# Kernel tuning notes

Measured on AMD Instinct MI355X. Metric: run time of the kernel, lower is better.

The kernel has to match this reference:

```python
import math
import jax, jax.numpy as jnp
import numpy as np

DIM = 768
TARGET_DIM = 1024  # next power of two >= DIM


def _hadamard_matrix(n: int) -> np.ndarray:
    # Sylvester construction, normalized by 1/sqrt(n)
    H = np.array([[1.0]], dtype=np.float32)
    while H.shape[0] < n:
        H = np.block([[H, H], [H, -H]])
    return H / math.sqrt(n)


_H = jnp.asarray(_hadamard_matrix(TARGET_DIM))  # [1024, 1024]


def setup_inputs() -> dict:
    key = jax.random.key(0)
    x = jax.random.normal(key, (16, 768, 56, 56), dtype=jnp.float32)
    return {"x": x}


def reference(x):
    B, C, Hs, Ws = x.shape  # C == DIM
    # [B, C, H, W] -> [B, H, W, C] -> [B*H*W, C]
    xr = jnp.transpose(x, (0, 2, 3, 1)).reshape(-1, DIM)
    # pad channel dim up to TARGET_DIM
    xp = jnp.pad(xr, ((0, 0), (0, TARGET_DIM - DIM)))
    y = xp @ _H.astype(x.dtype)           # [B*H*W, 1024]
    y = y[:, :DIM]                        # slice back to dim
    y = y.reshape(B, Hs, Ws, C)
    return jnp.transpose(y, (0, 3, 1, 2))  # [B, C, H, W]
```

## Files before the change

kernel.cpp:

```cpp
#include <hip/hip_runtime.h>


#define NSPAT 3136
#define TS    32
#define STQ   33
#define STI   529

static __device__ __forceinline__ float2 f2add(float2 a, float2 b) {
    return make_float2(a.x + b.x, a.y + b.y);
}
static __device__ __forceinline__ float2 f2sub(float2 a, float2 b) {
    return make_float2(a.x - b.x, a.y - b.y);
}

#define FWHT_STAGE(arr, D)                                   \
    _Pragma("unroll")                                        \
    for (int _b = 0; _b < 32; _b += 2 * (D)) {               \
        _Pragma("unroll")                                    \
        for (int _k = 0; _k < (D); ++_k) {                   \
            float2 _t = arr[_b + _k];                        \
            arr[_b + _k]       = f2add(_t, arr[_b + _k + (D)]); \
            arr[_b + _k + (D)] = f2sub(_t, arr[_b + _k + (D)]); \
        }                                                    \
    }

#define FWHT32(arr)       \
    FWHT_STAGE(arr, 16)   \
    FWHT_STAGE(arr, 8)    \
    FWHT_STAGE(arr, 4)    \
    FWHT_STAGE(arr, 2)    \
    FWHT_STAGE(arr, 1)

__global__ __launch_bounds__(256, 2)
void hadamard_c768_kernel(const float* __restrict__ x, float* __restrict__ y) {
    __shared__ float lds[24 * STI];

    const int t   = threadIdx.x;
    const int s2  = t & 15;
    const int g   = t >> 4;
    const int bid = blockIdx.x;
    const int b   = bid / (NSPAT / TS);
    const int s0  = (bid % (NSPAT / TS)) * TS;

    const int base = b * 768 * NSPAT + s0 + 2 * s2;
    const float* xb = x + base;
    float*       yb = y + base;

    float2 a0[32], a1[32];
    #pragma unroll
    for (int j = 0; j < 32; ++j)
        a0[j] = *(const float2*)(xb + (32 * g + j) * NSPAT);
    FWHT32(a0)

    const bool twoRows = (g < 8);
    if (twoRows) {
        #pragma unroll
        for (int j = 0; j < 32; ++j)
            a1[j] = *(const float2*)(xb + (32 * (g + 16) + j) * NSPAT);
        FWHT32(a1)
    }

    #pragma unroll
    for (int round = 0; round < 2; ++round) {
        const int qbase = 16 * round;

        {
            float* p = lds + g * STI + 2 * s2;
            #pragma unroll
            for (int qq = 0; qq < 16; ++qq) {
                p[qq * STQ]     = a0[qbase + qq].x;
                p[qq * STQ + 1] = a0[qbase + qq].y;
            }
            if (twoRows) {
                float* p1 = lds + (g + 16) * STI + 2 * s2;
                #pragma unroll
                for (int qq = 0; qq < 16; ++qq) {
                    p1[qq * STQ]     = a1[qbase + qq].x;
                    p1[qq * STQ + 1] = a1[qbase + qq].y;
                }
            }
        }
        __syncthreads();

        {
            float2 w[32];
            const float* p = lds + g * STQ + 2 * s2;
            #pragma unroll
            for (int i = 0; i < 24; ++i)
                w[i] = make_float2(p[i * STI], p[i * STI + 1]);

            #pragma unroll
            for (int i = 0; i < 8; ++i) {
                float2 tt = w[i];
                w[i]      = f2add(tt, w[i + 16]);
                w[i + 16] = f2sub(tt, w[i + 16]);
            }
            #pragma unroll
            for (int i = 8; i < 16; ++i)
                w[i + 16] = w[i];

            FWHT_STAGE(w, 8)
            FWHT_STAGE(w, 4)
            FWHT_STAGE(w, 2)
            FWHT_STAGE(w, 1)

            const int q = qbase + g;
            #pragma unroll
            for (int pp = 0; pp < 24; ++pp) {
                float2 v = w[pp];
                v.x *= 0.03125f;
                v.y *= 0.03125f;
                *(float2*)(yb + (32 * pp + q) * NSPAT) = v;
            }
        }
        if (round == 0)
            __syncthreads();
    }
}

extern "C" void kernel_launch(void* const* d_in, const int* in_sizes, int n_in,
                              void* d_out, int out_size, void* d_ws, size_t ws_size,
                              hipStream_t stream) {
    const float* x = (const float*)d_in[0];
    float*       y = (float*)d_out;
    const int nblocks = 16 * (NSPAT / TS);
    hadamard_c768_kernel<<<dim3(nblocks), dim3(256), 0, stream>>>(x, y);
}
```

Measured before the change: 272.6 us.

## Use 512 threads per block with one row group each and nontemporal scalar stores

Blocks grow from 256 to 512 threads. Each of 24 active 16-lane groups loads and transforms one 32-channel row group, which removes the uneven two-row-group work of the old layout. The second stage now uses scalar floats: each thread handles one spatial column for one q, and the output goes through nontemporal stores. This raises occupancy and balances work, at the cost of a quarter of the threads sitting idle in the first phase and narrower scalar stores in place of float2 stores.

```diff
diff --git a/kernel.cpp b/kernel.cpp
--- a/kernel.cpp
+++ b/kernel.cpp
@@ -13,7 +13,7 @@
     return make_float2(a.x - b.x, a.y - b.y);
 }
 
-#define FWHT_STAGE(arr, D)                                   \
+#define FWHT_STAGE2(arr, D)                                  \
     _Pragma("unroll")                                        \
     for (int _b = 0; _b < 32; _b += 2 * (D)) {               \
         _Pragma("unroll")                                    \
@@ -24,96 +24,92 @@
         }                                                    \
     }
 
-#define FWHT32(arr)       \
-    FWHT_STAGE(arr, 16)   \
-    FWHT_STAGE(arr, 8)    \
-    FWHT_STAGE(arr, 4)    \
-    FWHT_STAGE(arr, 2)    \
-    FWHT_STAGE(arr, 1)
+#define FWHT32_2(arr)      \
+    FWHT_STAGE2(arr, 16)   \
+    FWHT_STAGE2(arr, 8)    \
+    FWHT_STAGE2(arr, 4)    \
+    FWHT_STAGE2(arr, 2)    \
+    FWHT_STAGE2(arr, 1)
 
-__global__ __launch_bounds__(256, 2)
+#define FWHT_STAGE1(arr, D)                                  \
+    _Pragma("unroll")                                        \
+    for (int _b = 0; _b < 32; _b += 2 * (D)) {               \
+        _Pragma("unroll")                                    \
+        for (int _k = 0; _k < (D); ++_k) {                   \
+            float _t = arr[_b + _k];                         \
+            arr[_b + _k]       = _t + arr[_b + _k + (D)];    \
+            arr[_b + _k + (D)] = _t - arr[_b + _k + (D)];    \
+        }                                                    \
+    }
+
+__global__ __launch_bounds__(512, 5)
 void hadamard_c768_kernel(const float* __restrict__ x, float* __restrict__ y) {
     __shared__ float lds[24 * STI];
 
     const int t   = threadIdx.x;
-    const int s2  = t & 15;
-    const int g   = t >> 4;
     const int bid = blockIdx.x;
     const int b   = bid / (NSPAT / TS);
     const int s0  = (bid % (NSPAT / TS)) * TS;
+    const int base = b * 768 * NSPAT + s0;
 
-    const int base = b * 768 * NSPAT + s0 + 2 * s2;
-    const float* xb = x + base;
-    float*       yb = y + base;
+    const int g  = t >> 4;
+    const int ln = t & 15;
 
-    float2 a0[32], a1[32];
-    #pragma unroll
-    for (int j = 0; j < 32; ++j)
-        a0[j] = *(const float2*)(xb + (32 * g + j) * NSPAT);
-    FWHT32(a0)
-
-    const bool twoRows = (g < 8);
-    if (twoRows) {
+    float2 a[32];
+    const bool active = (g < 24);
+    if (active) {
+        const float* xb = x + base + 2 * ln;
         #pragma unroll
         for (int j = 0; j < 32; ++j)
-            a1[j] = *(const float2*)(xb + (32 * (g + 16) + j) * NSPAT);
-        FWHT32(a1)
+            a[j] = *(const float2*)(xb + (32 * g + j) * NSPAT);
+        FWHT32_2(a)
     }
 
+    const int q16 = t >> 5;
+    const int s   = t & 31;
+
     #pragma unroll
-    for (int round = 0; round < 2; ++round) {
-        const int qbase = 16 * round;
-
-        {
-            float* p = lds + g * STI + 2 * s2;
+    for (int r = 0; r < 2; ++r) {
+        if (active) {
+            float* p = lds + g * STI + 2 * ln;
             #pragma unroll
             for (int qq = 0; qq < 16; ++qq) {
-                p[qq * STQ]     = a0[qbase + qq].x;
-                p[qq * STQ + 1] = a0[qbase + qq].y;
-            }
-            if (twoRows) {
-                float* p1 = lds + (g + 16) * STI + 2 * s2;
-                #pragma unroll
-                for (int qq = 0; qq < 16; ++qq) {
-                    p1[qq * STQ]     = a1[qbase + qq].x;
-                    p1[qq * STQ + 1] = a1[qbase + qq].y;
-                }
+                p[qq * STQ]     = a[16 * r + qq].x;
+                p[qq * STQ + 1] = a[16 * r + qq].y;
             }
         }
         __syncthreads();
 
         {
-            float2 w[32];
-            const float* p = lds + g * STQ + 2 * s2;
+            float w[32];
+            const float* p = lds + q16 * STQ + s;
             #pragma unroll
             for (int i = 0; i < 24; ++i)
-                w[i] = make_float2(p[i * STI], p[i * STI + 1]);
+                w[i] = p[i * STI];
 
             #pragma unroll
             for (int i = 0; i < 8; ++i) {
-                float2 tt = w[i];
-                w[i]      = f2add(tt, w[i + 16]);
-                w[i + 16] = f2sub(tt, w[i + 16]);
+                float tt  = w[i];
+                w[i]      = tt + w[i + 16];
+                w[i + 16] = tt - w[i + 16];
             }
             #pragma unroll
             for (int i = 8; i < 16; ++i)
                 w[i + 16] = w[i];
 
-            FWHT_STAGE(w, 8)
-            FWHT_STAGE(w, 4)
-            FWHT_STAGE(w, 2)
-            FWHT_STAGE(w, 1)
+            FWHT_STAGE1(w, 8)
+            FWHT_STAGE1(w, 4)
+            FWHT_STAGE1(w, 2)
+            FWHT_STAGE1(w, 1)
 
-            const int q = qbase + g;
+            const int q = 16 * r + q16;
+            float* yb = y + base + s;
             #pragma unroll
-            for (int pp = 0; pp < 24; ++pp) {
-                float2 v = w[pp];
-                v.x *= 0.03125f;
-                v.y *= 0.03125f;
-                *(float2*)(yb + (32 * pp + q) * NSPAT) = v;
-            }
+            for (int pp = 0; pp < 24; ++pp)
+                __builtin_nontemporal_store(w[pp] * 0.03125f,
+                                            yb + (32 * pp + q) * NSPAT);
         }
-        if (round == 0)
+        if (r == 0)
             __syncthreads();
     }
 }
@@ -124,5 +120,5 @@
     const float* x = (const float*)d_in[0];
     float*       y = (float*)d_out;
     const int nblocks = 16 * (NSPAT / TS);
-    hadamard_c768_kernel<<<dim3(nblocks), dim3(256), 0, stream>>>(x, y);
+    hadamard_c768_kernel<<<dim3(nblocks), dim3(512), 0, stream>>>(x, y);
 }
```

Result: no change. 267.7 us (-1.8%).
